# Kernel tuning notes

Measured on AMD Instinct MI355X. Metric: run time of the kernel, lower is better.

The kernel has to match this reference:

```python
import jax, jax.numpy as jnp
import numpy as np

NM, C_IN, T, V = 256, 64, 128, 21
C_OUT = 64
N_CONVS = 3  # forward only uses convs[0..2]
EPS_BN = 1e-5


def _build_edges(nm, t):
    # replicates get_hi(): 6x6 incidence (transposed), tiled over NM*T graphs
    inc = np.array([[1, 0, 0, 0, 1, 0],
                    [1, 1, 0, 0, 0, 1],
                    [1, 0, 1, 0, 0, 1],
                    [1, 0, 0, 1, 0, 0],
                    [1, 0, 0, 0, 1, 0],
                    [0, 1, 1, 0, 0, 1]], dtype=np.int64).T
    r_idx, c_idx = np.nonzero(inc)  # row-major order, matches torch nonzero
    g = nm * t                      # num_graphs
    nnz = len(r_idx)                # 14
    row = np.tile(r_idx, g) + np.repeat(np.arange(g), nnz) * 6   # targets (edge-node ids)
    col = np.tile(c_idx, g) + np.repeat(np.arange(g), nnz) * 21  # sources (vertex ids)
    return jnp.asarray(col, jnp.int32), jnp.asarray(row, jnp.int32)


def setup_inputs() -> dict:
    key = jax.random.key(0)
    ks = jax.random.split(key, 8)
    x = jax.random.normal(ks[0], (NM, C_IN, T, V), dtype=jnp.float32)
    src, dst = _build_edges(NM, T)
    s_in = 1.0 / np.sqrt(C_IN)
    s_att = 1.0 / np.sqrt(C_OUT)
    Wl = jax.random.normal(ks[1], (N_CONVS, C_OUT, C_IN), jnp.float32) * s_in
    bl = jnp.zeros((N_CONVS, C_OUT), jnp.float32)
    Wr = jax.random.normal(ks[2], (N_CONVS, C_OUT, C_IN), jnp.float32) * s_in
    br = jnp.zeros((N_CONVS, C_OUT), jnp.float32)
    att = jax.random.normal(ks[3], (N_CONVS, C_OUT), jnp.float32) * s_att
    bias = jnp.zeros((N_CONVS, C_OUT), jnp.float32)
    gamma = jnp.full((C_OUT,), 1e-6, jnp.float32)  # bn_init(self.bn, 1e-6)
    beta = jnp.zeros((C_OUT,), jnp.float32)
    return {"x": x, "src": src, "dst": dst, "Wl": Wl, "bl": bl, "Wr": Wr,
            "br": br, "att": att, "bias": bias, "gamma": gamma, "beta": beta}


def _gatv2(feat, src_all, dst_all, valid, Wl, bl, Wr, br, att, bias, n):
    # GATv2Conv, heads=1: e_ij = att . LeakyReLU(Wl x_j + Wr x_i); softmax over dst
    xl = feat @ Wl.T + bl           # [N, Cout]
    xr = feat @ Wr.T + br           # [N, Cout]
    msg = xl[src_all]               # [E, Cout]
    e = jax.nn.leaky_relu(msg + xr[dst_all], 0.2) @ att  # [E]
    e = jnp.where(valid, e, -1e9)   # removed self-loops excluded
    m = jax.ops.segment_max(e, dst_all, num_segments=n)
    a = jnp.exp(e - m[dst_all]) * valid
    denom = jax.ops.segment_sum(a, dst_all, num_segments=n)
    a = a / denom[dst_all]
    return jax.ops.segment_sum(a[:, None] * msg, dst_all, num_segments=n) + bias


def reference(x, src, dst, Wl, bl, Wr, br, att, bias, gamma, beta):
    nm, c, t, v = x.shape
    n = nm * t * v
    feat = jnp.transpose(x, (0, 2, 3, 1)).reshape(n, c)  # '(nm t v) c'
    # PyG GATv2: remove existing self-loops, then add self-loops for all N nodes
    loop = jnp.arange(n, dtype=src.dtype)
    src_all = jnp.concatenate([src, loop])
    dst_all = jnp.concatenate([dst, loop])
    valid = jnp.concatenate([src != dst, jnp.ones((n,), bool)])
    y = None
    for i in range(N_CONVS):
        z = _gatv2(feat, src_all, dst_all, valid,
                   Wl[i], bl[i], Wr[i], br[i], att[i], bias[i], n)
        y = z if y is None else y + z
    y = y.reshape(nm, C_OUT, t, v)  # matches torch .view on node-major buffer
    # BatchNorm2d (eval, running mean 0 / var 1), gamma initialized to 1e-6
    y = y / jnp.sqrt(1.0 + EPS_BN) * gamma[None, :, None, None] + beta[None, :, None, None]
    return jax.nn.relu(y + x)  # residual identity (in_channels == out_channels)
```

## Files before the change

### kernel.cpp

```cpp
#include <hip/hip_runtime.h>
#include <hip/hip_bf16.h>

#define NMSLICE 2688
#define NMELEMS 172032
#define NNODE   688128
#define NDST    196608
#define BNRS    0.9999950000374996f

typedef __attribute__((ext_vector_type(8))) _Float16 half8;
typedef __attribute__((ext_vector_type(2))) _Float16 half2v;
typedef __attribute__((ext_vector_type(4))) unsigned uintx4;
typedef __attribute__((ext_vector_type(4))) float  floatx4;

__device__ __forceinline__ short h2s(float f) {
    union { _Float16 h; short s; } c;
    c.h = (_Float16)f;
    return c.s;
}
__device__ __forceinline__ half2v shfl_h2(half2v v, int srcLane) {
    int iv = __builtin_bit_cast(int, v);
    iv = __shfl(iv, srcLane, 64);
    return __builtin_bit_cast(half2v, iv);
}

__global__ void __launch_bounds__(256) prep_weights(
    const float* __restrict__ Wl, const float* __restrict__ Wr,
    const float* __restrict__ bl, const float* __restrict__ br,
    const float* __restrict__ bias, const float* __restrict__ att,
    short* __restrict__ wfrag, float* __restrict__ csum,
    float* __restrict__ bsum_p, float* __restrict__ bl_p, float* __restrict__ br_p,
    short* __restrict__ att_p)
{
    const int task = blockIdx.x * 256 + threadIdx.x;
    const int lane = task & 63;
    const int ks   = (task >> 6) & 1;
    const int nt   = (task >> 7) & 3;
    const int m    = task >> 9;
    const int co = nt * 16 + (lane & 15);
    const int k0 = ks * 32 + (lane >> 4) * 8;
    short v[8];
    if (m < 6) {
        const int cv = m >> 1;
        const float* W = (m & 1) ? (Wr + cv * 4096) : (Wl + cv * 4096);
        #pragma unroll
        for (int j = 0; j < 8; ++j) v[j] = h2s(W[co * 64 + k0 + j]);
    } else {
        #pragma unroll
        for (int j = 0; j < 8; ++j)
            v[j] = h2s(Wl[co*64 + k0 + j] + Wl[4096 + co*64 + k0 + j] + Wl[8192 + co*64 + k0 + j]);
    }
    #pragma unroll
    for (int j = 0; j < 8; ++j) wfrag[task * 8 + j] = v[j];

    if (blockIdx.x == 0 && threadIdx.x < 192) {
        const int t  = threadIdx.x;
        const int cv = t / 64, ch = t % 64;
        const int ct = ch >> 4, r = ch & 15;
        const int pidx = (cv * 4 + (r >> 2)) * 16 + ct * 4 + (r & 3);
        att_p[pidx] = h2s(att[t]);
        bl_p[pidx] = bl[t];
        br_p[pidx] = br[t];
        if (t < 64) {
            const int p0 = ((r >> 2)) * 16 + ct * 4 + (r & 3);
            bsum_p[p0] = bias[t] + bias[64 + t] + bias[128 + t];
            csum[t] = bl[t] + bl[64+t] + bl[128+t] + bias[t] + bias[64+t] + bias[128+t];
        }
    }
}

__global__ void __launch_bounds__(256) gat_heavy(
    const float* __restrict__ x,
    const short* __restrict__ wfrag,
    const float* __restrict__ bl_p, const float* __restrict__ br_p,
    const short* __restrict__ att_p, const float* __restrict__ bsum_p,
    const float* __restrict__ gamma, const float* __restrict__ beta,
    float* __restrict__ out)
{
    __shared__ short F[4][32 * 64];

    const int lane = threadIdx.x & 63;
    const int wave = threadIdx.x >> 6;
    const int sbid = ((blockIdx.x & 7) << 9) + (blockIdx.x >> 3);
    const int W  = sbid * 4 + wave;
    const int n0 = W * 12;
    const int s0 = W * 42;

    const int nmD = n0 / NMSLICE, rmD = n0 - nmD * NMSLICE;
    const int nmS = s0 / NMSLICE, rmS = s0 - nmS * NMSLICE;

    #pragma unroll
    for (int i = 0; i < 3; ++i) {
        const int task = i * 64 + lane;
        const int r  = task % 24;
        const int k8 = task / 24;
        const float* bp;
        if (r < 12) {
            bp = x + (size_t)nmD * NMELEMS + rmD + r;
        } else {
            const int s = r - 12;
            const int gl = s >= 6 ? 1 : 0;
            bp = x + (size_t)nmS * NMELEMS + rmS + gl * 21 + (s - gl * 6);
        }
        short v[8];
        #pragma unroll
        for (int j = 0; j < 8; ++j) v[j] = h2s(bp[(size_t)(k8 * 8 + j) * NMSLICE]);
        const int sr = (r < 12) ? r : r + 4;
        *reinterpret_cast<half8*>(&F[wave][sr * 64 + ((k8 ^ (sr & 7)) << 3)]) =
            *reinterpret_cast<half8*>(v);
    }

    const int l15 = lane & 15, l4 = lane >> 4;

    half8 aA[2][2];
    #pragma unroll
    for (int t = 0; t < 2; ++t) {
        const int arow = t * 16 + l15;
        #pragma unroll
        for (int ks = 0; ks < 2; ++ks)
            aA[t][ks] = *reinterpret_cast<const half8*>(
                &F[wave][arow * 64 + (((ks * 4 + l4) ^ (arow & 7)) << 3)]);
    }

    const int i15 = l15;
    const bool act = i15 < 12;
    const int gl = (i15 >= 6) ? 1 : 0;
    const int rr = i15 - gl * 6;
    const int sjbase = (lane & 48) + gl * 6;
    const unsigned long long TBL =
        31ull | (34ull << 8) | (36ull << 16) | (8ull << 24) | (17ull << 32) | (38ull << 40);
    unsigned mask = (unsigned)((TBL >> (rr * 8)) & 63u);
    if (W == 0 && gl == 0) mask &= ~(1u << rr);

    half2v yacc2[8];
    #pragma unroll
    for (int j = 0; j < 8; ++j) yacc2[j] = half2v{ (_Float16)0, (_Float16)0 };

    for (int cv = 0; cv < 3; ++cv) {
        half2v xlT0h[8], xlT1h[8], xrh[8];
        #pragma unroll
        for (int ct = 0; ct < 4; ++ct) {
            const short* wbL = wfrag + (size_t)(((cv * 2    ) * 4 + ct) * 2) * 512;
            const short* wbR = wfrag + (size_t)(((cv * 2 + 1) * 4 + ct) * 2) * 512;
            half8 wl0 = *reinterpret_cast<const half8*>(wbL + lane * 8);
            half8 wl1 = *reinterpret_cast<const half8*>(wbL + 512 + lane * 8);
            half8 wr0 = *reinterpret_cast<const half8*>(wbR + lane * 8);
            half8 wr1 = *reinterpret_cast<const half8*>(wbR + 512 + lane * 8);
            floatx4 biL = *reinterpret_cast<const floatx4*>(bl_p + (cv * 4 + l4) * 16 + ct * 4);
            floatx4 biR = *reinterpret_cast<const floatx4*>(br_p + (cv * 4 + l4) * 16 + ct * 4);
            floatx4 a0 = biL, a1 = biL, ar = biR;
            a0 = __builtin_amdgcn_mfma_f32_16x16x32_f16(wl0, aA[0][0], a0, 0, 0, 0);
            a0 = __builtin_amdgcn_mfma_f32_16x16x32_f16(wl1, aA[0][1], a0, 0, 0, 0);
            a1 = __builtin_amdgcn_mfma_f32_16x16x32_f16(wl0, aA[1][0], a1, 0, 0, 0);
            a1 = __builtin_amdgcn_mfma_f32_16x16x32_f16(wl1, aA[1][1], a1, 0, 0, 0);
            ar = __builtin_amdgcn_mfma_f32_16x16x32_f16(wr0, aA[0][0], ar, 0, 0, 0);
            ar = __builtin_amdgcn_mfma_f32_16x16x32_f16(wr1, aA[0][1], ar, 0, 0, 0);
            xlT0h[ct*2  ] = half2v{ (_Float16)a0[0], (_Float16)a0[1] };
            xlT0h[ct*2+1] = half2v{ (_Float16)a0[2], (_Float16)a0[3] };
            xlT1h[ct*2  ] = half2v{ (_Float16)a1[0], (_Float16)a1[1] };
            xlT1h[ct*2+1] = half2v{ (_Float16)a1[2], (_Float16)a1[3] };
            xrh [ct*2  ] = half2v{ (_Float16)ar[0], (_Float16)ar[1] };
            xrh [ct*2+1] = half2v{ (_Float16)ar[2], (_Float16)ar[3] };
        }

        if (act) {
            half2v a2[8];
            {
                const uintx4* ap = reinterpret_cast<const uintx4*>(att_p + (cv * 4 + l4) * 16);
                uintx4 v0 = ap[0], v1 = ap[1];
                #pragma unroll
                for (int j = 0; j < 4; ++j) {
                    a2[j]     = __builtin_bit_cast(half2v, v0[j]);
                    a2[4 + j] = __builtin_bit_cast(half2v, v1[j]);
                }
            }
            const half2v c02 = { (_Float16)0.2f, (_Float16)0.2f };
            float denom;
            half2v o2[8];
            {
                half2v s = { (_Float16)0, (_Float16)0 };
                #pragma unroll
                for (int j = 0; j < 8; ++j) {
                    half2v z = xlT0h[j] + xrh[j];
                    z = __builtin_elementwise_max(z, c02 * z);
                    s += a2[j] * z;
                }
                float e = (float)s[0] + (float)s[1];
                e += __shfl_xor(e, 16);
                e += __shfl_xor(e, 32);
                float w = __expf(e);
                denom = w;
                half2v w2 = { (_Float16)w, (_Float16)w };
                #pragma unroll
                for (int j = 0; j < 8; ++j) o2[j] = w2 * xlT0h[j];
            }
            #pragma unroll
            for (int c = 0; c < 6; ++c) {
                const int srcLane = sjbase + c;
                half2v m2[8];
                #pragma unroll
                for (int j = 0; j < 8; ++j) m2[j] = shfl_h2(xlT1h[j], srcLane);
                half2v s = { (_Float16)0, (_Float16)0 };
                #pragma unroll
                for (int j = 0; j < 8; ++j) {
                    half2v z = m2[j] + xrh[j];
                    z = __builtin_elementwise_max(z, c02 * z);
                    s += a2[j] * z;
                }
                float e = (float)s[0] + (float)s[1];
                e += __shfl_xor(e, 16);
                e += __shfl_xor(e, 32);
                float w = (mask & (1u << c)) ? __expf(e) : 0.f;
                denom += w;
                half2v w2 = { (_Float16)w, (_Float16)w };
                #pragma unroll
                for (int j = 0; j < 8; ++j) o2[j] += w2 * m2[j];
            }
            const _Float16 invh = (_Float16)(1.0f / denom);
            const half2v inv2 = { invh, invh };
            #pragma unroll
            for (int j = 0; j < 8; ++j) yacc2[j] += inv2 * o2[j];
        }
    }

    if (act) {
        const int rm = rmD + i15;
        const int cobn = rm / 42;
        const float sc = gamma[cobn] * BNRS;
        const float bt = beta[cobn];
        const size_t nb = (size_t)(n0 + i15) * 64;
        #pragma unroll
        for (int ct = 0; ct < 4; ++ct) {
            const size_t a0 = nb + ct * 16 + l4 * 4;
            floatx4 bs4 = *reinterpret_cast<const floatx4*>(bsum_p + l4 * 16 + ct * 4);
            floatx4 xv = *reinterpret_cast<const floatx4*>(x + a0);
            floatx4 ov;
            #pragma unroll
            for (int q = 0; q < 4; ++q) {
                const float yv = (float)yacc2[ct * 2 + (q >> 1)][q & 1];
                float val = fmaf(yv + bs4[q], sc, bt) + xv[q];
                ov[q] = fmaxf(val, 0.f);
            }
            *reinterpret_cast<floatx4*>(out + a0) = ov;
        }
    }
}

__global__ void __launch_bounds__(256) gat_light(
    const float* __restrict__ x,
    const short* __restrict__ wfrag,
    const float* __restrict__ csum,
    const float* __restrict__ gamma, const float* __restrict__ beta,
    float* __restrict__ out)
{
    __shared__ short F[256 * 64];

    const int t  = threadIdx.x;
    const int n0 = NDST + blockIdx.x * 256;

    {
        const int node = n0 + t;
        const int nm = node / NMSLICE;
        const int rm = node - nm * NMSLICE;
        const float* bp = x + (size_t)nm * NMELEMS + rm;
        #pragma unroll
        for (int k8 = 0; k8 < 8; ++k8) {
            short v[8];
            #pragma unroll
            for (int j = 0; j < 8; ++j) v[j] = h2s(bp[(size_t)(k8 * 8 + j) * NMSLICE]);
            *reinterpret_cast<half8*>(&F[t * 64 + ((k8 ^ (t & 7)) << 3)]) =
                *reinterpret_cast<half8*>(v);
        }
    }
    __syncthreads();

    const int wave = t >> 6, lane = t & 63;
    const int l15 = lane & 15, l4 = lane >> 4;
    const int rm0 = n0 % NMSLICE;
    #pragma unroll
    for (int ti = 0; ti < 16; ++ti) {
        const int tile = wave * 16 + ti;
        const int mt = tile >> 2, nt = tile & 3;
        const int co = nt * 16 + l15;
        const float bi = csum[co];
        floatx4 acc = { bi, bi, bi, bi };
        const short* wbase = wfrag + (size_t)((6 * 4 + nt) * 2) * 512;
        const int arow = mt * 16 + l15;
        #pragma unroll
        for (int ks = 0; ks < 2; ++ks) {
            half8 bfr = *reinterpret_cast<const half8*>(wbase + ks * 512 + lane * 8);
            const int k8 = ks * 4 + l4;
            half8 afr = *reinterpret_cast<const half8*>(
                &F[arow * 64 + ((k8 ^ (arow & 7)) << 3)]);
            acc = __builtin_amdgcn_mfma_f32_16x16x32_f16(afr, bfr, acc, 0, 0, 0);
        }
        #pragma unroll
        for (int qq = 0; qq < 4; ++qq) {
            const int row = mt * 16 + l4 * 4 + qq;
            int rm = rm0 + row; if (rm >= NMSLICE) rm -= NMSLICE;
            const int cobn = (rm * 64 + co) / NMSLICE;
            const size_t fi = (size_t)(n0 + row) * 64 + co;
            const float val = fmaf(acc[qq], gamma[cobn] * BNRS, beta[cobn]) + x[fi];
            out[fi] = fmaxf(val, 0.f);
        }
    }
}

extern "C" void kernel_launch(void* const* d_in, const int* in_sizes, int n_in,
                              void* d_out, int out_size, void* d_ws, size_t ws_size,
                              hipStream_t stream) {
    const float* x     = (const float*)d_in[0];
    const float* Wl    = (const float*)d_in[3];
    const float* bl    = (const float*)d_in[4];
    const float* Wr    = (const float*)d_in[5];
    const float* br    = (const float*)d_in[6];
    const float* att   = (const float*)d_in[7];
    const float* bias  = (const float*)d_in[8];
    const float* gamma = (const float*)d_in[9];
    const float* beta  = (const float*)d_in[10];
    float* out = (float*)d_out;

    char* ws = (char*)d_ws;
    short* wfrag  = (short*)ws;
    float* csum   = (float*)(ws + 57344);
    float* bsum_p = (float*)(ws + 57600);
    float* bl_p   = (float*)(ws + 57856);
    float* br_p   = (float*)(ws + 58624);
    short* att_p  = (short*)(ws + 59392);

    hipLaunchKernelGGL(prep_weights, dim3(14), dim3(256), 0, stream,
                       Wl, Wr, bl, br, bias, att, wfrag, csum, bsum_p, bl_p, br_p, att_p);
    hipLaunchKernelGGL(gat_heavy, dim3(4096), dim3(256), 0, stream,
                       x, wfrag, bl_p, br_p, att_p, bsum_p, gamma, beta, out);
    hipLaunchKernelGGL(gat_light, dim3(1920), dim3(256), 0, stream,
                       x, wfrag, csum, gamma, beta, out);
}
```

Before: 188.6 us.

## Split the three GATv2 convs across waves in gat_heavy with LDS reduction

Before, each wave processed one 12-node group and looped over all three convolutions serially. Now each block handles one group, with three waves each computing one convolution. The waves share the staged input tile in LDS, and partial outputs are summed through an LDS buffer before one wave runs the epilogue. This gives more parallelism and shortens each wave's serial chain, at the cost of two block barriers, extra LDS traffic, and four times as many smaller blocks.

Measured after the change: 201.6 us. 6.9% more time.

```diff
diff --git a/kernel.cpp b/kernel.cpp
--- a/kernel.cpp
+++ b/kernel.cpp
@@ -68,7 +68,7 @@
     }
 }
 
-__global__ void __launch_bounds__(256) gat_heavy(
+__global__ void __launch_bounds__(192) gat_heavy(
     const float* __restrict__ x,
     const short* __restrict__ wfrag,
     const float* __restrict__ bl_p, const float* __restrict__ br_p,
@@ -76,23 +76,22 @@
     const float* __restrict__ gamma, const float* __restrict__ beta,
     float* __restrict__ out)
 {
-    __shared__ short F[4][32 * 64];
-
-    const int lane = threadIdx.x & 63;
-    const int wave = threadIdx.x >> 6;
-    const int sbid = ((blockIdx.x & 7) << 9) + (blockIdx.x >> 3);
-    const int W  = sbid * 4 + wave;
-    const int n0 = W * 12;
-    const int s0 = W * 42;
+    __shared__ short F[32 * 64];
+    __shared__ float Y[2][16][68];
+
+    const int tid  = threadIdx.x;
+    const int lane = tid & 63;
+    const int cv   = tid >> 6;
+    const int gp = ((blockIdx.x & 7) << 11) + (blockIdx.x >> 3);
+    const int n0 = gp * 12;
+    const int s0 = gp * 42;
 
     const int nmD = n0 / NMSLICE, rmD = n0 - nmD * NMSLICE;
     const int nmS = s0 / NMSLICE, rmS = s0 - nmS * NMSLICE;
 
-    #pragma unroll
-    for (int i = 0; i < 3; ++i) {
-        const int task = i * 64 + lane;
-        const int r  = task % 24;
-        const int k8 = task / 24;
+    {
+        const int r  = tid % 24;
+        const int k8 = tid / 24;
         const float* bp;
         if (r < 12) {
             bp = x + (size_t)nmD * NMELEMS + rmD + r;
@@ -105,9 +104,10 @@
         #pragma unroll
         for (int j = 0; j < 8; ++j) v[j] = h2s(bp[(size_t)(k8 * 8 + j) * NMSLICE]);
         const int sr = (r < 12) ? r : r + 4;
-        *reinterpret_cast<half8*>(&F[wave][sr * 64 + ((k8 ^ (sr & 7)) << 3)]) =
+        *reinterpret_cast<half8*>(&F[sr * 64 + ((k8 ^ (sr & 7)) << 3)]) =
             *reinterpret_cast<half8*>(v);
     }
+    __syncthreads();
 
     const int l15 = lane & 15, l4 = lane >> 4;
 
@@ -118,7 +118,7 @@
         #pragma unroll
         for (int ks = 0; ks < 2; ++ks)
             aA[t][ks] = *reinterpret_cast<const half8*>(
-                &F[wave][arow * 64 + (((ks * 4 + l4) ^ (arow & 7)) << 3)]);
+                &F[arow * 64 + (((ks * 4 + l4) ^ (arow & 7)) << 3)]);
     }
 
     const int i15 = l15;
@@ -129,13 +129,13 @@
     const unsigned long long TBL =
         31ull | (34ull << 8) | (36ull << 16) | (8ull << 24) | (17ull << 32) | (38ull << 40);
     unsigned mask = (unsigned)((TBL >> (rr * 8)) & 63u);
-    if (W == 0 && gl == 0) mask &= ~(1u << rr);
+    if (gp == 0 && gl == 0) mask &= ~(1u << rr);
 
     half2v yacc2[8];
     #pragma unroll
     for (int j = 0; j < 8; ++j) yacc2[j] = half2v{ (_Float16)0, (_Float16)0 };
 
-    for (int cv = 0; cv < 3; ++cv) {
+    {
         half2v xlT0h[8], xlT1h[8], xrh[8];
         #pragma unroll
         for (int ct = 0; ct < 4; ++ct) {
@@ -222,7 +222,18 @@
         }
     }
 
-    if (act) {
+    if (cv != 0) {
+        #pragma unroll
+        for (int ct = 0; ct < 4; ++ct) {
+            floatx4 pv;
+            #pragma unroll
+            for (int q = 0; q < 4; ++q)
+                pv[q] = (float)yacc2[ct * 2 + (q >> 1)][q & 1];
+            *reinterpret_cast<floatx4*>(&Y[cv - 1][l15][ct * 16 + l4 * 4]) = pv;
+        }
+    }
+    __syncthreads();
+    if (cv == 0 && act) {
         const int rm = rmD + i15;
         const int cobn = rm / 42;
         const float sc = gamma[cobn] * BNRS;
@@ -231,12 +242,14 @@
         #pragma unroll
         for (int ct = 0; ct < 4; ++ct) {
             const size_t a0 = nb + ct * 16 + l4 * 4;
+            floatx4 y1 = *reinterpret_cast<const floatx4*>(&Y[0][l15][ct * 16 + l4 * 4]);
+            floatx4 y2 = *reinterpret_cast<const floatx4*>(&Y[1][l15][ct * 16 + l4 * 4]);
             floatx4 bs4 = *reinterpret_cast<const floatx4*>(bsum_p + l4 * 16 + ct * 4);
             floatx4 xv = *reinterpret_cast<const floatx4*>(x + a0);
             floatx4 ov;
             #pragma unroll
             for (int q = 0; q < 4; ++q) {
-                const float yv = (float)yacc2[ct * 2 + (q >> 1)][q & 1];
+                const float yv = (float)yacc2[ct * 2 + (q >> 1)][q & 1] + y1[q] + y2[q];
                 float val = fmaf(yv + bs4[q], sc, bt) + xv[q];
                 ov[q] = fmaxf(val, 0.f);
             }
@@ -329,7 +342,7 @@
 
     hipLaunchKernelGGL(prep_weights, dim3(14), dim3(256), 0, stream,
                        Wl, Wr, bl, br, bias, att, wfrag, csum, bsum_p, bl_p, br_p, att_p);
-    hipLaunchKernelGGL(gat_heavy, dim3(4096), dim3(256), 0, stream,
+    hipLaunchKernelGGL(gat_heavy, dim3(16384), dim3(192), 0, stream,
                        x, wfrag, bl_p, br_p, att_p, bsum_p, gamma, beta, out);
     hipLaunchKernelGGL(gat_light, dim3(1920), dim3(256), 0, stream,
                        x, wfrag, csum, gamma, beta, out);
```
